# Performance work log

Measured on AMD Instinct MI355X. Metric: run time of the kernel, lower is better.

Reference implementation:

```python
import jax, jax.numpy as jnp
import numpy as np

B, EMB, H, G, F, CH, O, OC, KT = 4096, 256, 256, 8, 96, 16, 5, 10, 5
BN_EPS = 1e-3


def _grouped_linear(x, w):
    # x: [B, I], w: [G, I//G, O//G] -> [B, O]
    b = x.shape[0]
    g, ig, og = w.shape
    xg = x.reshape(b, g, ig)
    return jnp.einsum('bgi,gio->bgo', xg, w).reshape(b, g * og)


def _gru_cell(x, h, k, rk, bias):
    # keras GRUCell, reset_after=True; gate order z, r, h; bias: [2, 3H]
    xs = x @ k + bias[0]
    hs = h @ rk + bias[1]
    xz, xr, xh = jnp.split(xs, 3, axis=-1)
    hz, hr, hh = jnp.split(hs, 3, axis=-1)
    z = jax.nn.sigmoid(xz + hz)
    r = jax.nn.sigmoid(xr + hr)
    cand = jnp.tanh(xh + r * hh)
    return z * h + (1.0 - z) * cand


def setup_inputs() -> dict:
    key = jax.random.key(0)
    ks = jax.random.split(key, 20)
    w = lambda i, shape: (jax.random.normal(ks[i], shape, dtype=jnp.float32) * 0.05)
    inp = {
        'emb': jax.random.normal(ks[0], (B, EMB), dtype=jnp.float32),
        'c0': jax.random.normal(ks[1], (B, 1, F, CH), dtype=jnp.float32),
        'df_dec_state': jax.random.normal(ks[2], (B, 2 * H), dtype=jnp.float32),
        'df_convp_buf': jax.random.normal(ks[3], (B, KT - 1, F, CH), dtype=jnp.float32),
        'w_in': w(4, (G, EMB // G, H // G)),
        'gru_k0': w(5, (H, 3 * H)),
        'gru_rk0': w(6, (H, 3 * H)),
        'gru_b0': w(7, (2, 3 * H)),
        'gru_k1': w(8, (H, 3 * H)),
        'gru_rk1': w(9, (H, 3 * H)),
        'gru_b1': w(10, (2, 3 * H)),
        'w_out': w(11, (G, H // G, (F * OC) // G)),
        'fc_a_w': w(12, (H, 1)),
        'fc_a_b': jnp.zeros((1,), dtype=jnp.float32),
        'conv_w': w(13, (KT, 1, CH // 2, OC)),  # grouped conv, groups=gcd(16,10)=2
        'pw_w': w(14, (OC, OC)),                # 1x1 pointwise, no bias
        'bn_gamma': jnp.ones((OC,), dtype=jnp.float32),
        'bn_beta': jnp.zeros((OC,), dtype=jnp.float32),
        'bn_mean': jnp.zeros((OC,), dtype=jnp.float32),
        'bn_var': jnp.ones((OC,), dtype=jnp.float32),
    }
    return inp


def reference(emb, c0, df_dec_state, df_convp_buf,
              w_in, gru_k0, gru_rk0, gru_b0, gru_k1, gru_rk1, gru_b1,
              w_out, fc_a_w, fc_a_b, conv_w, pw_w,
              bn_gamma, bn_beta, bn_mean, bn_var):
    b = emb.shape[0]
    # SqueezedGRUStep: grouped linear in-proj + ReLU
    x_in = jax.nn.relu(_grouped_linear(emb, w_in))  # [B, H]
    h0 = df_dec_state[:, :H]
    h1 = df_dec_state[:, H:]
    out0 = _gru_cell(x_in, h0, gru_k0, gru_rk0, gru_b0)
    out1 = _gru_cell(out0, h1, gru_k1, gru_rk1, gru_b1)
    new_state = jnp.concatenate([out0, out1], axis=-1)  # [B, 2H]
    c = out1 + x_in  # gru_skip = identity

    # causal conv step: concat buffer + current frame -> [B, KT, F, CH]
    x = jnp.concatenate([df_convp_buf, c0], axis=1)
    new_buf = x[:, 1:, :, :]
    # grouped conv (groups=2), kernel (KT,1), valid over the KT frames -> last frame
    xg = x.reshape(b, KT, F, 2, CH // 2)                 # [B,T,F,g,i]
    wg = conv_w.reshape(KT, CH // 2, 2, OC // 2)         # [T,i,g,o]
    y = jnp.einsum('btfgi,tigo->bfgo', xg, wg).reshape(b, F, OC)
    # separable pointwise 1x1 conv
    y = y @ pw_w
    # batch norm (inference) + relu
    inv = jax.lax.rsqrt(bn_var + BN_EPS)
    y = (y - bn_mean) * inv * bn_gamma + bn_beta
    c0_out = jax.nn.relu(y)                              # [B, F, OC]

    alpha = jax.nn.sigmoid(emb @ jnp.zeros_like(fc_a_w) + c @ fc_a_w + fc_a_b)  # [B,1]
    c_out = jnp.tanh(_grouped_linear(c, w_out)).reshape(b, F, OC)
    c_out = c_out + c0_out
    # DfOutputReshapeMF: [B,1,F,O*2] -> [B,O,1,F,2]
    coefs = c_out.reshape(b, 1, F, O, 2).transpose(0, 3, 1, 2, 4)
    return (coefs, alpha, new_state, new_buf)
```

## Files before the change

kernel.cpp:

```cpp
#include <hip/hip_runtime.h>

typedef unsigned short u16;
typedef __attribute__((ext_vector_type(8))) u16 u16x8;
typedef __attribute__((ext_vector_type(8))) __bf16 bf16x8;
typedef __attribute__((ext_vector_type(4))) float f32x4;

#define ALPHA_OFF   3932160
#define NST_OFF     3936256
#define NBUF_OFF    6033408

__device__ __forceinline__ u16 f2bf(float f) {
  unsigned u = __builtin_bit_cast(unsigned, f);
  u += 0x7fffu + ((u >> 16) & 1u);
  return (u16)(u >> 16);
}
__device__ __forceinline__ float bf2f(u16 v) {
  return __builtin_bit_cast(float, (unsigned)v << 16);
}
__device__ __forceinline__ float fsig(float x) { return 1.f / (1.f + __expf(-x)); }
__device__ __forceinline__ float ftanh(float x) {
  x = fminf(15.f, fmaxf(-15.f, x));
  float e = __expf(2.f * x);
  return (e - 1.f) / (e + 1.f);
}
__device__ __forceinline__ f32x4 mfma16(u16x8 a, u16x8 b, f32x4 c) {
  return __builtin_amdgcn_mfma_f32_16x16x32_bf16(
      __builtin_bit_cast(bf16x8, a), __builtin_bit_cast(bf16x8, b), c, 0, 0, 0);
}
__device__ __forceinline__ void gload16(const void* g, void* l) {
  __builtin_amdgcn_global_load_lds(
      (const __attribute__((address_space(1))) void*)g,
      (__attribute__((address_space(3))) void*)l, 16, 0, 0);
}

__global__ __launch_bounds__(256) void wprep_kernel(
    const float* __restrict__ gk0, const float* __restrict__ grk0,
    const float* __restrict__ gk1, const float* __restrict__ grk1,
    u16* __restrict__ W2) {
  __shared__ u16 tl[64][65];
  int nb = blockIdx.x, kb = blockIdx.y, L = blockIdx.z;
  const float* src = (kb < 4) ? (L ? gk1 : gk0) : (L ? grk1 : grk0);
  int kbase = (kb & 3) * 64;
  u16* dst = W2 + (size_t)L * 768 * 512;
  int tid = threadIdx.x, c = tid & 63, r4 = tid >> 6;
  for (int rr = 0; rr < 64; rr += 4) {
    int k = kbase + rr + r4, n = nb * 64 + c;
    tl[rr + r4][c] = f2bf(src[(size_t)k * 768 + n]);
  }
  __syncthreads();
  for (int rr = 0; rr < 64; rr += 4) {
    int n = nb * 64 + rr + r4, k = kb * 64 + c;
    dst[(size_t)n * 512 + k] = tl[c][rr + r4];
  }
}

__global__ __launch_bounds__(256) void w3prep_kernel(
    const float* __restrict__ w_out, u16* __restrict__ W3) {
  int g = blockIdx.x, tid = threadIdx.x;
  for (int i = tid; i < 4096; i += 256) {
    int col = i >> 5, k = i & 31;
    float v = (col < 120) ? w_out[(size_t)g * 3840 + k * 120 + col] : 0.f;
    W3[(size_t)g * 4096 + i] = f2bf(v);
  }
}

__global__ __launch_bounds__(256) void prep_kernel(
    const float* __restrict__ emb, const float* __restrict__ dec,
    const float* __restrict__ w_in, u16* __restrict__ A0, u16* __restrict__ A1) {
  __shared__ float el[4][256];
  int tid = threadIdx.x, rowBase = blockIdx.x * 4;
  {
    int r = tid >> 6, c4 = tid & 63;
    *(float4*)&el[r][c4 * 4] = ((const float4*)emb)[(size_t)(rowBase + r) * 64 + c4];
  }
  int g = tid >> 5, o = tid & 31;
  float wr[32];
#pragma unroll
  for (int i = 0; i < 32; ++i) wr[i] = w_in[g * 1024 + i * 32 + o];
  __syncthreads();
#pragma unroll
  for (int r = 0; r < 4; ++r) {
    float acc = 0.f;
#pragma unroll
    for (int i = 0; i < 32; ++i) acc += el[r][g * 32 + i] * wr[i];
    A0[(size_t)(rowBase + r) * 512 + tid] = f2bf(fmaxf(acc, 0.f));
  }
  const float4* d4 = (const float4*)dec;
#pragma unroll
  for (int j = 0; j < 2; ++j) {
    int idx = tid + j * 256;
    int r = idx >> 7, c4 = idx & 127;
    float4 v = d4[(size_t)(rowBase + r) * 128 + c4];
    ushort4 q;
    q.x = f2bf(v.x); q.y = f2bf(v.y); q.z = f2bf(v.z); q.w = f2bf(v.w);
    u16* dst = (c4 < 64) ? A0 + (size_t)(rowBase + r) * 512 + 256 + c4 * 4
                         : A1 + (size_t)(rowBase + r) * 512 + 256 + (c4 - 64) * 4;
    *(ushort4*)dst = q;
  }
}

template <int LAYER>
__global__ __launch_bounds__(256) void gru_kernel(
    const u16* __restrict__ Ain,
    const u16* __restrict__ W2,
    const float* __restrict__ dec,
    const float* __restrict__ bias,
    float* __restrict__ nst,
    u16* __restrict__ a1out,
    const u16* __restrict__ xbf,
    u16* __restrict__ c_bf) {
  __shared__ __align__(16) u16 lsA[2][32][32];
  __shared__ __align__(16) u16 lsB[2][3][64][32];
  int tid = threadIdx.x, lane = tid & 63, wave = tid >> 6;
  int m0 = lane & 15, quad = lane >> 4;
  int rowBase = blockIdx.x * 32, jz = blockIdx.y * 64, cw = wave * 16;
  f32x4 acc[4][2];
#pragma unroll
  for (int gi = 0; gi < 4; ++gi)
#pragma unroll
    for (int rb = 0; rb < 2; ++rb) acc[gi][rb] = (f32x4){0.f, 0.f, 0.f, 0.f};

  int rS = tid >> 2, qS = tid & 3;
  auto stage = [&](int buf, int k0) {
    if (tid < 128)
      gload16(Ain + (size_t)(rowBase + rS) * 512 + k0 + qS * 8,
              &lsA[buf][rS][qS * 8]);
#pragma unroll
    for (int g = 0; g < 3; ++g)
      gload16(W2 + (size_t)(g * 256 + jz + rS) * 512 + k0 + qS * 8,
              &lsB[buf][g][rS][qS * 8]);
  };

  stage(0, 0);
  for (int step = 0; step < 16; ++step) {
    __syncthreads();
    if (step < 15) stage((step & 1) ^ 1, (step + 1) * 32);
    int cur = step & 1;
    u16x8 av[2], bv[3];
#pragma unroll
    for (int rb = 0; rb < 2; ++rb)
      av[rb] = *(const u16x8*)&lsA[cur][rb * 16 + m0][quad * 8];
#pragma unroll
    for (int g = 0; g < 3; ++g)
      bv[g] = *(const u16x8*)&lsB[cur][g][cw + m0][quad * 8];
#pragma unroll
    for (int rb = 0; rb < 2; ++rb) {
      acc[0][rb] = mfma16(av[rb], bv[0], acc[0][rb]);
      acc[1][rb] = mfma16(av[rb], bv[1], acc[1][rb]);
    }
    if (step < 8) {
#pragma unroll
      for (int rb = 0; rb < 2; ++rb) acc[2][rb] = mfma16(av[rb], bv[2], acc[2][rb]);
    } else {
#pragma unroll
      for (int rb = 0; rb < 2; ++rb) acc[3][rb] = mfma16(av[rb], bv[2], acc[3][rb]);
    }
  }

  int col = jz + cw + m0;
  float bz = bias[col] + bias[768 + col];
  float br = bias[256 + col] + bias[1024 + col];
  float bxh = bias[512 + col];
  float bhh = bias[1280 + col];
  const int hoff = LAYER ? 256 : 0;
#pragma unroll
  for (int rb = 0; rb < 2; ++rb) {
#pragma unroll
    for (int i = 0; i < 4; ++i) {
      int row = rowBase + rb * 16 + quad * 4 + i;
      float h = dec[(size_t)row * 512 + hoff + col];
      float z = fsig(acc[0][rb][i] + bz);
      float r = fsig(acc[1][rb][i] + br);
      float cand = ftanh(acc[2][rb][i] + bxh + r * (acc[3][rb][i] + bhh));
      float o = z * h + (1.f - z) * cand;
      nst[(size_t)row * 512 + hoff + col] = o;
      if (LAYER == 0) {
        a1out[(size_t)row * 512 + col] = f2bf(o);
      } else {
        float c = o + bf2f(xbf[(size_t)row * 512 + col]);
        c_bf[(size_t)row * 256 + col] = f2bf(c);
      }
    }
  }
}

__global__ __launch_bounds__(256) void wout_kernel(
    const u16* __restrict__ c_bf, const u16* __restrict__ W3,
    float* __restrict__ outc) {
  __shared__ __align__(16) u16 lsA[64][32];
  __shared__ __align__(16) u16 lsB[128][32];
  int tid = threadIdx.x, lane = tid & 63, wave = tid >> 6;
  int m0 = lane & 15, quad = lane >> 4;
  int rowBase = blockIdx.x * 64, g = blockIdx.y;
  {
    int r = tid >> 2, q = tid & 3;
    gload16(c_bf + (size_t)(rowBase + r) * 256 + g * 32 + q * 8, &lsA[r][q * 8]);
    gload16(W3 + (size_t)g * 4096 + (size_t)r * 32 + q * 8, &lsB[r][q * 8]);
    gload16(W3 + (size_t)g * 4096 + (size_t)(64 + r) * 32 + q * 8, &lsB[64 + r][q * 8]);
  }
  __syncthreads();
  int cw = wave * 32;
  f32x4 acc[4][2];
#pragma unroll
  for (int rb = 0; rb < 4; ++rb)
#pragma unroll
    for (int cb = 0; cb < 2; ++cb) acc[rb][cb] = (f32x4){0.f, 0.f, 0.f, 0.f};
  u16x8 bv[2];
#pragma unroll
  for (int cb = 0; cb < 2; ++cb)
    bv[cb] = *(const u16x8*)&lsB[cw + cb * 16 + m0][quad * 8];
#pragma unroll
  for (int rb = 0; rb < 4; ++rb) {
    u16x8 av = *(const u16x8*)&lsA[rb * 16 + m0][quad * 8];
#pragma unroll
    for (int cb = 0; cb < 2; ++cb) acc[rb][cb] = mfma16(av, bv[cb], acc[rb][cb]);
  }
#pragma unroll
  for (int cb = 0; cb < 2; ++cb) {
    int cg = cw + cb * 16 + m0;
    if (cg < 120) {
#pragma unroll
      for (int rb = 0; rb < 4; ++rb)
#pragma unroll
        for (int i = 0; i < 4; ++i)
          outc[(size_t)(rowBase + rb * 16 + quad * 4 + i) * 960 + g * 120 + cg] =
              ftanh(acc[rb][cb][i]);
    }
  }
}

__global__ __launch_bounds__(192) void head_kernel(
    const float* __restrict__ convp, const float* __restrict__ c0,
    const u16* __restrict__ c_bf,
    const float* __restrict__ conv_w, const float* __restrict__ pw_w,
    const float* __restrict__ bng, const float* __restrict__ bnb,
    const float* __restrict__ bnm, const float* __restrict__ bnv,
    const float* __restrict__ fca_w, const float* __restrict__ fca_b,
    float* __restrict__ outp) {
  __shared__ __align__(16) float cw2[640];
  __shared__ float pws[100];
  __shared__ float bsc[10], bsh[10];
  __shared__ float ybuf[96][11];
  __shared__ float ared[3];
  int tid = threadIdx.x, lane = tid & 63, wave = tid >> 6;
  int b = blockIdx.x;
  int f = tid >> 1, half = tid & 1;
  const float4* cp4 = (const float4*)convp;
  const float4* c04 = (const float4*)c0;
  float4* nb4 = (float4*)(outp + NBUF_OFF);

  size_t sbase = (size_t)b * 1536 + f * 4 + half * 2;
  size_t cbase = (size_t)b * 384 + f * 4 + half * 2;
  float4 xa0 = cp4[sbase];         float4 xb0 = cp4[sbase + 1];
  float4 xa1 = cp4[sbase + 384];   float4 xb1 = cp4[sbase + 385];
  float4 xa2 = cp4[sbase + 768];   float4 xb2 = cp4[sbase + 769];
  float4 xa3 = cp4[sbase + 1152];  float4 xb3 = cp4[sbase + 1153];
  float4 xa4 = c04[cbase];         float4 xb4 = c04[cbase + 1];
  float tmp[5];
#pragma unroll
  for (int k = 0; k < 5; ++k) {
    int u = tid + k * 192;
    tmp[k] = outp[(size_t)b * 960 + (u % 96) * 10 + (u / 96)];
  }
  float ap = bf2f(c_bf[(size_t)b * 256 + tid]) * fca_w[tid];
  if (tid < 64) ap += bf2f(c_bf[(size_t)b * 256 + 192 + tid]) * fca_w[192 + tid];

  for (int i = tid; i < 400; i += 192) {
    int t = i / 80, rr = (i % 80) / 10, h = (i % 10) / 5, j = i % 5;
    cw2[((t * 8 + rr) * 2 + h) * 8 + j] = conv_w[i];
  }
  if (tid < 100) pws[tid] = pw_w[tid];
  if (tid < 10) {
    float s = bng[tid] * rsqrtf(bnv[tid] + 1e-3f);
    bsc[tid] = s;
    bsh[tid] = bnb[tid] - bnm[tid] * s;
  }
  nb4[sbase] = xa1;         nb4[sbase + 1] = xb1;
  nb4[sbase + 384] = xa2;   nb4[sbase + 385] = xb2;
  nb4[sbase + 768] = xa3;   nb4[sbase + 769] = xb3;
  nb4[sbase + 1152] = xa4;  nb4[sbase + 1153] = xb4;
#pragma unroll
  for (int off = 32; off > 0; off >>= 1) ap += __shfl_down(ap, off, 64);
  if (lane == 0) ared[wave] = ap;
  __syncthreads();
  float a5[5] = {0.f, 0.f, 0.f, 0.f, 0.f};
#define CI(XF, T, I)                                                        \
  {                                                                         \
    const float* wp = &cw2[(((T) * 8 + (I)) * 2 + half) * 8];               \
    float4 w03 = *(const float4*)wp;                                        \
    float w4 = wp[4];                                                       \
    a5[0] += (XF) * w03.x; a5[1] += (XF) * w03.y; a5[2] += (XF) * w03.z;    \
    a5[3] += (XF) * w03.w; a5[4] += (XF) * w4;                              \
  }
#define CTAP(VA, VB, T)                                                     \
  CI(VA.x, T, 0) CI(VA.y, T, 1) CI(VA.z, T, 2) CI(VA.w, T, 3)               \
  CI(VB.x, T, 4) CI(VB.y, T, 5) CI(VB.z, T, 6) CI(VB.w, T, 7)
  CTAP(xa0, xb0, 0)
  CTAP(xa1, xb1, 1)
  CTAP(xa2, xb2, 2)
  CTAP(xa3, xb3, 3)
  CTAP(xa4, xb4, 4)
#undef CTAP
#undef CI
#pragma unroll
  for (int j = 0; j < 5; ++j) ybuf[f][half * 5 + j] = a5[j];
  __syncthreads();
  if (tid == 0)
    outp[ALPHA_OFF + b] = fsig(ared[0] + ared[1] + ared[2] + fca_b[0]);
  float vals[5];
#pragma unroll
  for (int k = 0; k < 5; ++k) {
    int u = tid + k * 192;
    int p = u / 96, ff = u % 96;
    float y2 = 0.f;
#pragma unroll
    for (int j = 0; j < 10; ++j) y2 += ybuf[ff][j] * pws[j * 10 + p];
    vals[k] = fmaxf(y2 * bsc[p] + bsh[p], 0.f) + tmp[k];
  }
#pragma unroll
  for (int k = 0; k < 5; ++k) {
    int u = tid + k * 192;
    int p = u / 96, ff = u % 96;
    outp[(size_t)b * 960 + (p >> 1) * 192 + ff * 2 + (p & 1)] = vals[k];
  }
}

extern "C" void kernel_launch(void* const* d_in, const int* in_sizes, int n_in,
                              void* d_out, int out_size, void* d_ws, size_t ws_size,
                              hipStream_t stream) {
  const float* emb    = (const float*)d_in[0];
  const float* c0     = (const float*)d_in[1];
  const float* dec    = (const float*)d_in[2];
  const float* convp  = (const float*)d_in[3];
  const float* w_in   = (const float*)d_in[4];
  const float* gk0    = (const float*)d_in[5];
  const float* grk0   = (const float*)d_in[6];
  const float* gb0    = (const float*)d_in[7];
  const float* gk1    = (const float*)d_in[8];
  const float* grk1   = (const float*)d_in[9];
  const float* gb1    = (const float*)d_in[10];
  const float* w_out  = (const float*)d_in[11];
  const float* fca_w  = (const float*)d_in[12];
  const float* fca_b  = (const float*)d_in[13];
  const float* conv_w = (const float*)d_in[14];
  const float* pw_w   = (const float*)d_in[15];
  const float* bng    = (const float*)d_in[16];
  const float* bnb    = (const float*)d_in[17];
  const float* bnm    = (const float*)d_in[18];
  const float* bnv    = (const float*)d_in[19];
  float* out = (float*)d_out;
  char* ws = (char*)d_ws;
  u16* A0   = (u16*)(ws + 0);
  u16* A1   = (u16*)(ws + 4194304);
  u16* c_bf = (u16*)(ws + 8388608);
  u16* W2   = (u16*)(ws + 10485760);
  u16* W3   = (u16*)(ws + 12058624);

  wprep_kernel<<<dim3(12, 8, 2), 256, 0, stream>>>(gk0, grk0, gk1, grk1, W2);
  w3prep_kernel<<<dim3(8), 256, 0, stream>>>(w_out, W3);
  prep_kernel<<<dim3(1024), 256, 0, stream>>>(emb, dec, w_in, A0, A1);
  gru_kernel<0><<<dim3(128, 4), 256, 0, stream>>>(A0, W2, dec, gb0,
                                                  out + NST_OFF, A1, nullptr, nullptr);
  gru_kernel<1><<<dim3(128, 4), 256, 0, stream>>>(A1, W2 + 768 * 512, dec, gb1,
                                                  out + NST_OFF, nullptr, A0, c_bf);
  wout_kernel<<<dim3(64, 8), 256, 0, stream>>>(c_bf, W3, out);
  head_kernel<<<dim3(4096), 192, 0, stream>>>(convp, c0, c_bf, conv_w, pw_w,
                                              bng, bnb, bnm, bnv, fca_w, fca_b, out);
}
```

Before: 312.6 us.

## Fuse weight and activation prep kernels; fold output grouped linear into head kernel

The GRU weight transpose and the input-projection prep now run as one kernel launch with block-index dispatch. The w_out bf16 pre-pack kernel and the MFMA-based wout_kernel are removed. The grouped output linear plus tanh is instead computed per batch row inside head_kernel with fp32 FMAs that read w_out straight from global memory. This drops three launches and the intermediate write and read-back of the output tensor. In exchange, the output projection moves from matrix cores to scalar FMAs, and each of the 4096 blocks rereads the weights, relying on cache hits.

```diff
diff --git a/kernel.cpp b/kernel.cpp
--- a/kernel.cpp
+++ b/kernel.cpp
@@ -33,69 +33,60 @@
       (__attribute__((address_space(3))) void*)l, 16, 0, 0);
 }
 
-__global__ __launch_bounds__(256) void wprep_kernel(
+__global__ __launch_bounds__(256) void prep_all_kernel(
+    const float* __restrict__ emb, const float* __restrict__ dec,
+    const float* __restrict__ w_in,
     const float* __restrict__ gk0, const float* __restrict__ grk0,
     const float* __restrict__ gk1, const float* __restrict__ grk1,
-    u16* __restrict__ W2) {
-  __shared__ u16 tl[64][65];
-  int nb = blockIdx.x, kb = blockIdx.y, L = blockIdx.z;
-  const float* src = (kb < 4) ? (L ? gk1 : gk0) : (L ? grk1 : grk0);
-  int kbase = (kb & 3) * 64;
-  u16* dst = W2 + (size_t)L * 768 * 512;
-  int tid = threadIdx.x, c = tid & 63, r4 = tid >> 6;
-  for (int rr = 0; rr < 64; rr += 4) {
-    int k = kbase + rr + r4, n = nb * 64 + c;
-    tl[rr + r4][c] = f2bf(src[(size_t)k * 768 + n]);
-  }
-  __syncthreads();
-  for (int rr = 0; rr < 64; rr += 4) {
-    int n = nb * 64 + rr + r4, k = kb * 64 + c;
-    dst[(size_t)n * 512 + k] = tl[c][rr + r4];
-  }
-}
-
-__global__ __launch_bounds__(256) void w3prep_kernel(
-    const float* __restrict__ w_out, u16* __restrict__ W3) {
-  int g = blockIdx.x, tid = threadIdx.x;
-  for (int i = tid; i < 4096; i += 256) {
-    int col = i >> 5, k = i & 31;
-    float v = (col < 120) ? w_out[(size_t)g * 3840 + k * 120 + col] : 0.f;
-    W3[(size_t)g * 4096 + i] = f2bf(v);
-  }
-}
-
-__global__ __launch_bounds__(256) void prep_kernel(
-    const float* __restrict__ emb, const float* __restrict__ dec,
-    const float* __restrict__ w_in, u16* __restrict__ A0, u16* __restrict__ A1) {
-  __shared__ float el[4][256];
-  int tid = threadIdx.x, rowBase = blockIdx.x * 4;
-  {
-    int r = tid >> 6, c4 = tid & 63;
-    *(float4*)&el[r][c4 * 4] = ((const float4*)emb)[(size_t)(rowBase + r) * 64 + c4];
-  }
-  int g = tid >> 5, o = tid & 31;
-  float wr[32];
-#pragma unroll
-  for (int i = 0; i < 32; ++i) wr[i] = w_in[g * 1024 + i * 32 + o];
-  __syncthreads();
-#pragma unroll
-  for (int r = 0; r < 4; ++r) {
-    float acc = 0.f;
-#pragma unroll
-    for (int i = 0; i < 32; ++i) acc += el[r][g * 32 + i] * wr[i];
-    A0[(size_t)(rowBase + r) * 512 + tid] = f2bf(fmaxf(acc, 0.f));
-  }
-  const float4* d4 = (const float4*)dec;
-#pragma unroll
-  for (int j = 0; j < 2; ++j) {
-    int idx = tid + j * 256;
-    int r = idx >> 7, c4 = idx & 127;
-    float4 v = d4[(size_t)(rowBase + r) * 128 + c4];
-    ushort4 q;
-    q.x = f2bf(v.x); q.y = f2bf(v.y); q.z = f2bf(v.z); q.w = f2bf(v.w);
-    u16* dst = (c4 < 64) ? A0 + (size_t)(rowBase + r) * 512 + 256 + c4 * 4
-                         : A1 + (size_t)(rowBase + r) * 512 + 256 + (c4 - 64) * 4;
-    *(ushort4*)dst = q;
+    u16* __restrict__ A0, u16* __restrict__ A1, u16* __restrict__ W2) {
+  int bi = blockIdx.x, tid = threadIdx.x;
+  if (bi < 192) {
+    __shared__ u16 tl[64][65];
+    int nb = bi % 12, kb = (bi / 12) % 8, L = bi / 96;
+    const float* src = (kb < 4) ? (L ? gk1 : gk0) : (L ? grk1 : grk0);
+    int kbase = (kb & 3) * 64;
+    u16* dst = W2 + (size_t)L * 768 * 512;
+    int c = tid & 63, r4 = tid >> 6;
+    for (int rr = 0; rr < 64; rr += 4) {
+      int k = kbase + rr + r4, n = nb * 64 + c;
+      tl[rr + r4][c] = f2bf(src[(size_t)k * 768 + n]);
+    }
+    __syncthreads();
+    for (int rr = 0; rr < 64; rr += 4) {
+      int n = nb * 64 + rr + r4, k = kb * 64 + c;
+      dst[(size_t)n * 512 + k] = tl[c][rr + r4];
+    }
+  } else {
+    __shared__ float el[4][256];
+    int rowBase = (bi - 192) * 4;
+    {
+      int r = tid >> 6, c4 = tid & 63;
+      *(float4*)&el[r][c4 * 4] = ((const float4*)emb)[(size_t)(rowBase + r) * 64 + c4];
+    }
+    int g = tid >> 5, o = tid & 31;
+    float wr[32];
+#pragma unroll
+    for (int i = 0; i < 32; ++i) wr[i] = w_in[g * 1024 + i * 32 + o];
+    __syncthreads();
+#pragma unroll
+    for (int r = 0; r < 4; ++r) {
+      float acc = 0.f;
+#pragma unroll
+      for (int i = 0; i < 32; ++i) acc += el[r][g * 32 + i] * wr[i];
+      A0[(size_t)(rowBase + r) * 512 + tid] = f2bf(fmaxf(acc, 0.f));
+    }
+    const float4* d4 = (const float4*)dec;
+#pragma unroll
+    for (int j = 0; j < 2; ++j) {
+      int idx = tid + j * 256;
+      int r = idx >> 7, c4 = idx & 127;
+      float4 v = d4[(size_t)(rowBase + r) * 128 + c4];
+      ushort4 q;
+      q.x = f2bf(v.x); q.y = f2bf(v.y); q.z = f2bf(v.z); q.w = f2bf(v.w);
+      u16* dst = (c4 < 64) ? A0 + (size_t)(rowBase + r) * 512 + 256 + c4 * 4
+                           : A1 + (size_t)(rowBase + r) * 512 + 256 + (c4 - 64) * 4;
+      *(ushort4*)dst = q;
+    }
   }
 }
 
@@ -184,51 +175,6 @@
   }
 }
 
-__global__ __launch_bounds__(256) void wout_kernel(
-    const u16* __restrict__ c_bf, const u16* __restrict__ W3,
-    float* __restrict__ outc) {
-  __shared__ __align__(16) u16 lsA[64][32];
-  __shared__ __align__(16) u16 lsB[128][32];
-  int tid = threadIdx.x, lane = tid & 63, wave = tid >> 6;
-  int m0 = lane & 15, quad = lane >> 4;
-  int rowBase = blockIdx.x * 64, g = blockIdx.y;
-  {
-    int r = tid >> 2, q = tid & 3;
-    gload16(c_bf + (size_t)(rowBase + r) * 256 + g * 32 + q * 8, &lsA[r][q * 8]);
-    gload16(W3 + (size_t)g * 4096 + (size_t)r * 32 + q * 8, &lsB[r][q * 8]);
-    gload16(W3 + (size_t)g * 4096 + (size_t)(64 + r) * 32 + q * 8, &lsB[64 + r][q * 8]);
-  }
-  __syncthreads();
-  int cw = wave * 32;
-  f32x4 acc[4][2];
-#pragma unroll
-  for (int rb = 0; rb < 4; ++rb)
-#pragma unroll
-    for (int cb = 0; cb < 2; ++cb) acc[rb][cb] = (f32x4){0.f, 0.f, 0.f, 0.f};
-  u16x8 bv[2];
-#pragma unroll
-  for (int cb = 0; cb < 2; ++cb)
-    bv[cb] = *(const u16x8*)&lsB[cw + cb * 16 + m0][quad * 8];
-#pragma unroll
-  for (int rb = 0; rb < 4; ++rb) {
-    u16x8 av = *(const u16x8*)&lsA[rb * 16 + m0][quad * 8];
-#pragma unroll
-    for (int cb = 0; cb < 2; ++cb) acc[rb][cb] = mfma16(av, bv[cb], acc[rb][cb]);
-  }
-#pragma unroll
-  for (int cb = 0; cb < 2; ++cb) {
-    int cg = cw + cb * 16 + m0;
-    if (cg < 120) {
-#pragma unroll
-      for (int rb = 0; rb < 4; ++rb)
-#pragma unroll
-        for (int i = 0; i < 4; ++i)
-          outc[(size_t)(rowBase + rb * 16 + quad * 4 + i) * 960 + g * 120 + cg] =
-              ftanh(acc[rb][cb][i]);
-    }
-  }
-}
-
 __global__ __launch_bounds__(192) void head_kernel(
     const float* __restrict__ convp, const float* __restrict__ c0,
     const u16* __restrict__ c_bf,
@@ -236,12 +182,14 @@
     const float* __restrict__ bng, const float* __restrict__ bnb,
     const float* __restrict__ bnm, const float* __restrict__ bnv,
     const float* __restrict__ fca_w, const float* __restrict__ fca_b,
+    const float* __restrict__ w_out,
     float* __restrict__ outp) {
   __shared__ __align__(16) float cw2[640];
   __shared__ float pws[100];
   __shared__ float bsc[10], bsh[10];
   __shared__ float ybuf[96][11];
   __shared__ float ared[3];
+  __shared__ float cl[8][33];
   int tid = threadIdx.x, lane = tid & 63, wave = tid >> 6;
   int b = blockIdx.x;
   int f = tid >> 1, half = tid & 1;
@@ -256,14 +204,14 @@
   float4 xa2 = cp4[sbase + 768];   float4 xb2 = cp4[sbase + 769];
   float4 xa3 = cp4[sbase + 1152];  float4 xb3 = cp4[sbase + 1153];
   float4 xa4 = c04[cbase];         float4 xb4 = c04[cbase + 1];
-  float tmp[5];
-#pragma unroll
-  for (int k = 0; k < 5; ++k) {
-    int u = tid + k * 192;
-    tmp[k] = outp[(size_t)b * 960 + (u % 96) * 10 + (u / 96)];
-  }
-  float ap = bf2f(c_bf[(size_t)b * 256 + tid]) * fca_w[tid];
-  if (tid < 64) ap += bf2f(c_bf[(size_t)b * 256 + 192 + tid]) * fca_w[192 + tid];
+  float cv = bf2f(c_bf[(size_t)b * 256 + tid]);
+  cl[tid >> 5][tid & 31] = cv;
+  float ap = cv * fca_w[tid];
+  if (tid < 64) {
+    float cv2 = bf2f(c_bf[(size_t)b * 256 + 192 + tid]);
+    cl[(192 + tid) >> 5][tid & 31] = cv2;
+    ap += cv2 * fca_w[192 + tid];
+  }
 
   for (int i = tid; i < 400; i += 192) {
     int t = i / 80, rr = (i % 80) / 10, h = (i % 10) / 5, j = i % 5;
@@ -283,6 +231,24 @@
   for (int off = 32; off > 0; off >>= 1) ap += __shfl_down(ap, off, 64);
   if (lane == 0) ared[wave] = ap;
   __syncthreads();
+
+  float a8[8] = {0.f, 0.f, 0.f, 0.f, 0.f, 0.f, 0.f, 0.f};
+  int gg = 0, o0 = 0;
+  if (tid < 120) {
+    gg = tid / 15; o0 = (tid % 15) * 8;
+    const float* wp = w_out + (size_t)gg * 3840 + o0;
+#pragma unroll
+    for (int k = 0; k < 32; ++k) {
+      float ck = cl[gg][k];
+      float4 wA = *(const float4*)(wp + k * 120);
+      float4 wB = *(const float4*)(wp + k * 120 + 4);
+      a8[0] += ck * wA.x; a8[1] += ck * wA.y;
+      a8[2] += ck * wA.z; a8[3] += ck * wA.w;
+      a8[4] += ck * wB.x; a8[5] += ck * wB.y;
+      a8[6] += ck * wB.z; a8[7] += ck * wB.w;
+    }
+  }
+
   float a5[5] = {0.f, 0.f, 0.f, 0.f, 0.f};
 #define CI(XF, T, I)                                                        \
   {                                                                         \
@@ -307,21 +273,17 @@
   __syncthreads();
   if (tid == 0)
     outp[ALPHA_OFF + b] = fsig(ared[0] + ared[1] + ared[2] + fca_b[0]);
-  float vals[5];
-#pragma unroll
-  for (int k = 0; k < 5; ++k) {
-    int u = tid + k * 192;
-    int p = u / 96, ff = u % 96;
-    float y2 = 0.f;
-#pragma unroll
-    for (int j = 0; j < 10; ++j) y2 += ybuf[ff][j] * pws[j * 10 + p];
-    vals[k] = fmaxf(y2 * bsc[p] + bsh[p], 0.f) + tmp[k];
-  }
-#pragma unroll
-  for (int k = 0; k < 5; ++k) {
-    int u = tid + k * 192;
-    int p = u / 96, ff = u % 96;
-    outp[(size_t)b * 960 + (p >> 1) * 192 + ff * 2 + (p & 1)] = vals[k];
+  if (tid < 120) {
+#pragma unroll
+    for (int m = 0; m < 8; ++m) {
+      int e = gg * 120 + o0 + m;
+      int ff = e / 10, p = e % 10;
+      float y2 = 0.f;
+#pragma unroll
+      for (int j = 0; j < 10; ++j) y2 += ybuf[ff][j] * pws[j * 10 + p];
+      float v = fmaxf(y2 * bsc[p] + bsh[p], 0.f) + ftanh(a8[m]);
+      outp[(size_t)b * 960 + (p >> 1) * 192 + ff * 2 + (p & 1)] = v;
+    }
   }
 }
 
@@ -354,16 +316,15 @@
   u16* A1   = (u16*)(ws + 4194304);
   u16* c_bf = (u16*)(ws + 8388608);
   u16* W2   = (u16*)(ws + 10485760);
-  u16* W3   = (u16*)(ws + 12058624);
-
-  wprep_kernel<<<dim3(12, 8, 2), 256, 0, stream>>>(gk0, grk0, gk1, grk1, W2);
-  w3prep_kernel<<<dim3(8), 256, 0, stream>>>(w_out, W3);
-  prep_kernel<<<dim3(1024), 256, 0, stream>>>(emb, dec, w_in, A0, A1);
+
+  prep_all_kernel<<<dim3(1216), 256, 0, stream>>>(emb, dec, w_in,
+                                                  gk0, grk0, gk1, grk1,
+                                                  A0, A1, W2);
   gru_kernel<0><<<dim3(128, 4), 256, 0, stream>>>(A0, W2, dec, gb0,
                                                   out + NST_OFF, A1, nullptr, nullptr);
   gru_kernel<1><<<dim3(128, 4), 256, 0, stream>>>(A1, W2 + 768 * 512, dec, gb1,
                                                   out + NST_OFF, nullptr, A0, c_bf);
-  wout_kernel<<<dim3(64, 8), 256, 0, stream>>>(c_bf, W3, out);
   head_kernel<<<dim3(4096), 192, 0, stream>>>(convp, c0, c_bf, conv_w, pw_w,
-                                              bng, bnb, bnm, bnv, fca_w, fca_b, out);
-}
+                                              bng, bnb, bnm, bnv, fca_w, fca_b,
+                                              w_out, out);
+}
```

After: 323.0 us. +3.3%, slower.

## Merge prep kernels, write wout in final layout, batch two rows per head block

Applied to the files above, without the earlier changes.

The three preparation kernels (GRU weight transpose, output-weight conversion, input projection) become one launch that dispatches on block index, which removes two kernel launches. The wout kernel now writes its tanh outputs straight into the final coefficient permutation, so the head kernel reads and writes contiguous strided elements instead of gathering and scattering through a transposed index. The head kernel handles two batch rows per 384-thread block, which halves the block count and shares the weight staging in shared memory across two rows. The risk is scattered stores from wout and extra shared-memory use per head block.

```diff
diff --git a/kernel.cpp b/kernel.cpp
--- a/kernel.cpp
+++ b/kernel.cpp
@@ -33,69 +33,69 @@
       (__attribute__((address_space(3))) void*)l, 16, 0, 0);
 }
 
-__global__ __launch_bounds__(256) void wprep_kernel(
+__global__ __launch_bounds__(256) void prep_all_kernel(
+    const float* __restrict__ emb, const float* __restrict__ dec,
+    const float* __restrict__ w_in,
     const float* __restrict__ gk0, const float* __restrict__ grk0,
     const float* __restrict__ gk1, const float* __restrict__ grk1,
-    u16* __restrict__ W2) {
-  __shared__ u16 tl[64][65];
-  int nb = blockIdx.x, kb = blockIdx.y, L = blockIdx.z;
-  const float* src = (kb < 4) ? (L ? gk1 : gk0) : (L ? grk1 : grk0);
-  int kbase = (kb & 3) * 64;
-  u16* dst = W2 + (size_t)L * 768 * 512;
-  int tid = threadIdx.x, c = tid & 63, r4 = tid >> 6;
-  for (int rr = 0; rr < 64; rr += 4) {
-    int k = kbase + rr + r4, n = nb * 64 + c;
-    tl[rr + r4][c] = f2bf(src[(size_t)k * 768 + n]);
-  }
-  __syncthreads();
-  for (int rr = 0; rr < 64; rr += 4) {
-    int n = nb * 64 + rr + r4, k = kb * 64 + c;
-    dst[(size_t)n * 512 + k] = tl[c][rr + r4];
-  }
-}
-
-__global__ __launch_bounds__(256) void w3prep_kernel(
-    const float* __restrict__ w_out, u16* __restrict__ W3) {
-  int g = blockIdx.x, tid = threadIdx.x;
-  for (int i = tid; i < 4096; i += 256) {
-    int col = i >> 5, k = i & 31;
-    float v = (col < 120) ? w_out[(size_t)g * 3840 + k * 120 + col] : 0.f;
-    W3[(size_t)g * 4096 + i] = f2bf(v);
-  }
-}
-
-__global__ __launch_bounds__(256) void prep_kernel(
-    const float* __restrict__ emb, const float* __restrict__ dec,
-    const float* __restrict__ w_in, u16* __restrict__ A0, u16* __restrict__ A1) {
-  __shared__ float el[4][256];
-  int tid = threadIdx.x, rowBase = blockIdx.x * 4;
-  {
-    int r = tid >> 6, c4 = tid & 63;
-    *(float4*)&el[r][c4 * 4] = ((const float4*)emb)[(size_t)(rowBase + r) * 64 + c4];
-  }
-  int g = tid >> 5, o = tid & 31;
-  float wr[32];
-#pragma unroll
-  for (int i = 0; i < 32; ++i) wr[i] = w_in[g * 1024 + i * 32 + o];
-  __syncthreads();
-#pragma unroll
-  for (int r = 0; r < 4; ++r) {
-    float acc = 0.f;
-#pragma unroll
-    for (int i = 0; i < 32; ++i) acc += el[r][g * 32 + i] * wr[i];
-    A0[(size_t)(rowBase + r) * 512 + tid] = f2bf(fmaxf(acc, 0.f));
-  }
-  const float4* d4 = (const float4*)dec;
-#pragma unroll
-  for (int j = 0; j < 2; ++j) {
-    int idx = tid + j * 256;
-    int r = idx >> 7, c4 = idx & 127;
-    float4 v = d4[(size_t)(rowBase + r) * 128 + c4];
-    ushort4 q;
-    q.x = f2bf(v.x); q.y = f2bf(v.y); q.z = f2bf(v.z); q.w = f2bf(v.w);
-    u16* dst = (c4 < 64) ? A0 + (size_t)(rowBase + r) * 512 + 256 + c4 * 4
-                         : A1 + (size_t)(rowBase + r) * 512 + 256 + (c4 - 64) * 4;
-    *(ushort4*)dst = q;
+    const float* __restrict__ w_out,
+    u16* __restrict__ A0, u16* __restrict__ A1, u16* __restrict__ W2,
+    u16* __restrict__ W3) {
+  int bi = blockIdx.x, tid = threadIdx.x;
+  if (bi < 192) {
+    __shared__ u16 tl[64][65];
+    int nb = bi % 12, kb = (bi / 12) % 8, L = bi / 96;
+    const float* src = (kb < 4) ? (L ? gk1 : gk0) : (L ? grk1 : grk0);
+    int kbase = (kb & 3) * 64;
+    u16* dst = W2 + (size_t)L * 768 * 512;
+    int c = tid & 63, r4 = tid >> 6;
+    for (int rr = 0; rr < 64; rr += 4) {
+      int k = kbase + rr + r4, n = nb * 64 + c;
+      tl[rr + r4][c] = f2bf(src[(size_t)k * 768 + n]);
+    }
+    __syncthreads();
+    for (int rr = 0; rr < 64; rr += 4) {
+      int n = nb * 64 + rr + r4, k = kb * 64 + c;
+      dst[(size_t)n * 512 + k] = tl[c][rr + r4];
+    }
+  } else if (bi < 200) {
+    int g = bi - 192;
+    for (int i = tid; i < 4096; i += 256) {
+      int col = i >> 5, k = i & 31;
+      float v = (col < 120) ? w_out[(size_t)g * 3840 + k * 120 + col] : 0.f;
+      W3[(size_t)g * 4096 + i] = f2bf(v);
+    }
+  } else {
+    __shared__ float el[4][256];
+    int rowBase = (bi - 200) * 4;
+    {
+      int r = tid >> 6, c4 = tid & 63;
+      *(float4*)&el[r][c4 * 4] = ((const float4*)emb)[(size_t)(rowBase + r) * 64 + c4];
+    }
+    int g = tid >> 5, o = tid & 31;
+    float wr[32];
+#pragma unroll
+    for (int i = 0; i < 32; ++i) wr[i] = w_in[g * 1024 + i * 32 + o];
+    __syncthreads();
+#pragma unroll
+    for (int r = 0; r < 4; ++r) {
+      float acc = 0.f;
+#pragma unroll
+      for (int i = 0; i < 32; ++i) acc += el[r][g * 32 + i] * wr[i];
+      A0[(size_t)(rowBase + r) * 512 + tid] = f2bf(fmaxf(acc, 0.f));
+    }
+    const float4* d4 = (const float4*)dec;
+#pragma unroll
+    for (int j = 0; j < 2; ++j) {
+      int idx = tid + j * 256;
+      int r = idx >> 7, c4 = idx & 127;
+      float4 v = d4[(size_t)(rowBase + r) * 128 + c4];
+      ushort4 q;
+      q.x = f2bf(v.x); q.y = f2bf(v.y); q.z = f2bf(v.z); q.w = f2bf(v.w);
+      u16* dst = (c4 < 64) ? A0 + (size_t)(rowBase + r) * 512 + 256 + c4 * 4
+                           : A1 + (size_t)(rowBase + r) * 512 + 256 + (c4 - 64) * 4;
+      *(ushort4*)dst = q;
+    }
   }
 }
 
@@ -219,17 +219,20 @@
   for (int cb = 0; cb < 2; ++cb) {
     int cg = cw + cb * 16 + m0;
     if (cg < 120) {
+      int e0 = g * 120 + cg;
+      int ff = e0 / 10, p = e0 % 10;
+      int fin = (p >> 1) * 192 + ff * 2 + (p & 1);
 #pragma unroll
       for (int rb = 0; rb < 4; ++rb)
 #pragma unroll
         for (int i = 0; i < 4; ++i)
-          outc[(size_t)(rowBase + rb * 16 + quad * 4 + i) * 960 + g * 120 + cg] =
+          outc[(size_t)(rowBase + rb * 16 + quad * 4 + i) * 960 + fin] =
               ftanh(acc[rb][cb][i]);
     }
   }
 }
 
-__global__ __launch_bounds__(192) void head_kernel(
+__global__ __launch_bounds__(384) void head_kernel(
     const float* __restrict__ convp, const float* __restrict__ c0,
     const u16* __restrict__ c_bf,
     const float* __restrict__ conv_w, const float* __restrict__ pw_w,
@@ -240,17 +243,18 @@
   __shared__ __align__(16) float cw2[640];
   __shared__ float pws[100];
   __shared__ float bsc[10], bsh[10];
-  __shared__ float ybuf[96][11];
-  __shared__ float ared[3];
+  __shared__ float ybuf[2][96][11];
+  __shared__ float ared[6];
   int tid = threadIdx.x, lane = tid & 63, wave = tid >> 6;
-  int b = blockIdx.x;
-  int f = tid >> 1, half = tid & 1;
+  int row = tid >= 192, t = tid - row * 192;
+  int brow = blockIdx.x * 2 + row;
+  int f = t >> 1, half = t & 1;
   const float4* cp4 = (const float4*)convp;
   const float4* c04 = (const float4*)c0;
   float4* nb4 = (float4*)(outp + NBUF_OFF);
 
-  size_t sbase = (size_t)b * 1536 + f * 4 + half * 2;
-  size_t cbase = (size_t)b * 384 + f * 4 + half * 2;
+  size_t sbase = (size_t)brow * 1536 + f * 4 + half * 2;
+  size_t cbase = (size_t)brow * 384 + f * 4 + half * 2;
   float4 xa0 = cp4[sbase];         float4 xb0 = cp4[sbase + 1];
   float4 xa1 = cp4[sbase + 384];   float4 xb1 = cp4[sbase + 385];
   float4 xa2 = cp4[sbase + 768];   float4 xb2 = cp4[sbase + 769];
@@ -258,16 +262,14 @@
   float4 xa4 = c04[cbase];         float4 xb4 = c04[cbase + 1];
   float tmp[5];
 #pragma unroll
-  for (int k = 0; k < 5; ++k) {
-    int u = tid + k * 192;
-    tmp[k] = outp[(size_t)b * 960 + (u % 96) * 10 + (u / 96)];
-  }
-  float ap = bf2f(c_bf[(size_t)b * 256 + tid]) * fca_w[tid];
-  if (tid < 64) ap += bf2f(c_bf[(size_t)b * 256 + 192 + tid]) * fca_w[192 + tid];
-
-  for (int i = tid; i < 400; i += 192) {
-    int t = i / 80, rr = (i % 80) / 10, h = (i % 10) / 5, j = i % 5;
-    cw2[((t * 8 + rr) * 2 + h) * 8 + j] = conv_w[i];
+  for (int k = 0; k < 5; ++k)
+    tmp[k] = outp[(size_t)brow * 960 + t + k * 192];
+  float ap = bf2f(c_bf[(size_t)brow * 256 + t]) * fca_w[t];
+  if (t < 64) ap += bf2f(c_bf[(size_t)brow * 256 + 192 + t]) * fca_w[192 + t];
+
+  for (int i = tid; i < 400; i += 384) {
+    int tt = i / 80, rr = (i % 80) / 10, h = (i % 10) / 5, j = i % 5;
+    cw2[((tt * 8 + rr) * 2 + h) * 8 + j] = conv_w[i];
   }
   if (tid < 100) pws[tid] = pw_w[tid];
   if (tid < 10) {
@@ -303,26 +305,23 @@
 #undef CTAP
 #undef CI
 #pragma unroll
-  for (int j = 0; j < 5; ++j) ybuf[f][half * 5 + j] = a5[j];
+  for (int j = 0; j < 5; ++j) ybuf[row][f][half * 5 + j] = a5[j];
   __syncthreads();
-  if (tid == 0)
-    outp[ALPHA_OFF + b] = fsig(ared[0] + ared[1] + ared[2] + fca_b[0]);
+  if (t == 0)
+    outp[ALPHA_OFF + brow] =
+        fsig(ared[row * 3] + ared[row * 3 + 1] + ared[row * 3 + 2] + fca_b[0]);
   float vals[5];
 #pragma unroll
   for (int k = 0; k < 5; ++k) {
-    int u = tid + k * 192;
-    int p = u / 96, ff = u % 96;
+    int p = k * 2 + half;
     float y2 = 0.f;
 #pragma unroll
-    for (int j = 0; j < 10; ++j) y2 += ybuf[ff][j] * pws[j * 10 + p];
+    for (int j = 0; j < 10; ++j) y2 += ybuf[row][f][j] * pws[j * 10 + p];
     vals[k] = fmaxf(y2 * bsc[p] + bsh[p], 0.f) + tmp[k];
   }
 #pragma unroll
-  for (int k = 0; k < 5; ++k) {
-    int u = tid + k * 192;
-    int p = u / 96, ff = u % 96;
-    outp[(size_t)b * 960 + (p >> 1) * 192 + ff * 2 + (p & 1)] = vals[k];
-  }
+  for (int k = 0; k < 5; ++k)
+    outp[(size_t)brow * 960 + t + k * 192] = vals[k];
 }
 
 extern "C" void kernel_launch(void* const* d_in, const int* in_sizes, int n_in,
@@ -356,14 +355,14 @@
   u16* W2   = (u16*)(ws + 10485760);
   u16* W3   = (u16*)(ws + 12058624);
 
-  wprep_kernel<<<dim3(12, 8, 2), 256, 0, stream>>>(gk0, grk0, gk1, grk1, W2);
-  w3prep_kernel<<<dim3(8), 256, 0, stream>>>(w_out, W3);
-  prep_kernel<<<dim3(1024), 256, 0, stream>>>(emb, dec, w_in, A0, A1);
+  prep_all_kernel<<<dim3(1224), 256, 0, stream>>>(emb, dec, w_in,
+                                                  gk0, grk0, gk1, grk1, w_out,
+                                                  A0, A1, W2, W3);
   gru_kernel<0><<<dim3(128, 4), 256, 0, stream>>>(A0, W2, dec, gb0,
                                                   out + NST_OFF, A1, nullptr, nullptr);
   gru_kernel<1><<<dim3(128, 4), 256, 0, stream>>>(A1, W2 + 768 * 512, dec, gb1,
                                                   out + NST_OFF, nullptr, A0, c_bf);
   wout_kernel<<<dim3(64, 8), 256, 0, stream>>>(c_bf, W3, out);
-  head_kernel<<<dim3(4096), 192, 0, stream>>>(convp, c0, c_bf, conv_w, pw_w,
+  head_kernel<<<dim3(2048), 384, 0, stream>>>(convp, c0, c_bf, conv_w, pw_w,
                                               bng, bnb, bnm, bnv, fca_w, fca_b, out);
 }
```

New measurement: 307.0 us. No clear change (-1.8%).
